# Optimization experiments

Measured on AMD Instinct MI355X. Metric: run time of the kernel, lower is better.

The kernel has to match this reference:

```python
import jax, jax.numpy as jnp
import numpy as np

STRIDE = 4
EPS = 1e-12  # guards sqrt grad at exactly-zero distance (weight[0] is all zeros)


def rbf_conv(x, w, stride=STRIDE):
    # x: (N, 1, H, W); w: (O, kh, kw). Computes per-window cdist to all O
    # prototype filters, then gauss RBF with std = unbiased std of the (N, O)
    # distance matrix at each window position (matches torch.std(dist)).
    O, kh, kw = w.shape
    patches = jax.lax.conv_general_dilated_patches(
        x, (kh, kw), (stride, stride), 'VALID')      # (N, kh*kw, oh, ow)
    p = jnp.transpose(patches, (0, 2, 3, 1))          # (N, oh, ow, P)
    wf = w.reshape(O, -1)                              # (O, P)
    d2 = (jnp.sum(p * p, -1)[..., None] + jnp.sum(wf * wf, -1)
          - 2.0 * jnp.einsum('nhwp,op->nhwo', p, wf))
    dist = jnp.sqrt(jnp.maximum(d2, 0.0) + EPS)       # (N, oh, ow, O)
    std = jnp.std(dist, axis=(0, 3), ddof=1, keepdims=True)  # per window pos
    out = jnp.exp(-0.5 * (dist / std) ** 2)           # gauss RBF
    return jnp.transpose(out, (0, 3, 1, 2))           # (N, O, oh, ow)


def crelu(x, b):
    return x * (x >= b).astype(x.dtype)


def sfm(x, shape, next_kernel, filt, alpha0=0.9):
    # get_RM: (N, C, h_in, w_in) -> (B, h, w, C) regrouping, then alpha-weighted
    # patch pooling over `filt`, emitting (B*h'*w', 1, kh_next, kw_next).
    h, w = shape
    f0, f1 = filt
    C = x.shape[1]
    rm = jnp.transpose(x, (0, 2, 3, 1)).reshape(-1, h, w, C)
    seq = jnp.arange(f0 * f1, dtype=x.dtype)[::-1]       # flipped sequence
    alpha = jnp.tile((alpha0 ** seq).reshape(f0, f1), (h // f0, w // f1))
    out = rm * alpha[None, :, :, None]
    out = out.reshape(-1, h // f0, f0, w // f1, f1, C).mean(axis=(2, 4))
    return out.reshape(-1, 1, *next_kernel)


def channel_forward(xc, w1, w2, w3, w4, cb):
    y = rbf_conv(xc, w1)                       # (B, 100, 6, 6)
    y = crelu(y, cb[0])
    y = sfm(y, (6, 6), (10, 10), (2, 2))       # (B*9, 1, 10, 10)
    y = rbf_conv(y, w2)                        # (B*9, 225, 1, 1)
    y = crelu(y, cb[1])
    y = sfm(y, (3, 3), (15, 15), (1, 3))       # (B*3, 1, 15, 15)
    y = rbf_conv(y, w3)                        # (B*3, 625, 1, 1)
    y = crelu(y, cb[2])
    y = sfm(y, (3, 1), (25, 25), (3, 1))       # (B, 1, 25, 25)
    y = rbf_conv(y, w4)                        # (B, 1225, 1, 1)
    y = crelu(y, cb[3])
    return y


def forward(x, w1, w2, w3, w4, fc_w, fc_b, crelu_bias):
    B = x.shape[0]
    feats = [channel_forward(x[:, c:c + 1], w1[c], w2[c], w3[c], w4[c], crelu_bias)
             for c in range(x.shape[1])]        # fixed loop over 3 color channels
    out = jnp.concatenate(feats, axis=1).reshape(B, -1)  # (B, 3*1225)
    return out @ fc_w.T + fc_b


def setup_inputs() -> dict:
    key = jax.random.key(0)
    ks = jax.random.split(key, 8)

    def kaiming_u(k, shape):
        fan_in = int(np.prod(shape[2:]))        # 1*kh*kw, matches torch
        bound = float(np.sqrt(1.0 / fan_in))    # kaiming_uniform(a=sqrt(5))
        w = jax.random.uniform(k, shape, jnp.float32, -bound, bound)
        return w.at[:, 0].set(0.0)              # torch init zeros filter 0

    B = 4096
    return {
        'x': jax.random.uniform(ks[0], (B, 3, 28, 28), jnp.float32),
        'w1': kaiming_u(ks[1], (3, 100, 5, 5)),
        'w2': kaiming_u(ks[2], (3, 225, 10, 10)),
        'w3': kaiming_u(ks[3], (3, 625, 15, 15)),
        'w4': kaiming_u(ks[4], (3, 1225, 25, 25)),
        'fc_w': jax.random.normal(ks[5], (10, 3 * 1225), jnp.float32) * 0.016,
        'fc_b': jnp.zeros((10,), jnp.float32),
        'crelu_bias': jnp.array([0.4, 0.1, 0.01, 0.01], jnp.float32),
    }


def reference(x, w1, w2, w3, w4, fc_w, fc_b, crelu_bias):
    return forward(x, w1, w2, w3, w4, fc_w, fc_b, crelu_bias)
```

## Files before the change

### kernel.cpp

```cpp
#include <hip/hip_runtime.h>


typedef unsigned short u16;
typedef short bf16x8 __attribute__((ext_vector_type(8)));
typedef float f32x4 __attribute__((ext_vector_type(4)));
typedef unsigned int u32;
typedef u32 u32x4 __attribute__((ext_vector_type(4)));

#define STRIPES 64
#define ACC_L2 0
#define ACC_L3 128
#define ACC_L4 256
#define ACC_TOTAL 384

__device__ __forceinline__ u16 f2bf(float f) {
  unsigned int u = __float_as_uint(f);
  unsigned int r = (u + 0x7fffu + ((u >> 16) & 1u)) >> 16;
  return (u16)r;
}
__device__ __forceinline__ float bf2f(u16 h) {
  return __uint_as_float(((unsigned int)h) << 16);
}
__device__ __forceinline__ u32 cvtpk_bf16(float a, float b) {
  u32 r;
  asm("v_cvt_pk_bf16_f32 %0, %1, %2" : "=v"(r) : "v"(a), "v"(b));
  return r;
}
__device__ __forceinline__ float fexp(float x) { return __expf(x); }
__device__ __forceinline__ float fsqrt(float x) { return __builtin_amdgcn_sqrtf(x); }
__device__ __forceinline__ void gload16(const void* g, const void* l) {
  __builtin_amdgcn_global_load_lds(
      (const __attribute__((address_space(1))) unsigned int*)g,
      (__attribute__((address_space(3))) unsigned int*)l, 16, 0, 0);
}

__global__ void zero_acc_kernel(double* __restrict__ acc, int n) {
  int i = blockIdx.x * blockDim.x + threadIdx.x;
  if (i < n) acc[i] = 0.0;
}

__global__ __launch_bounds__(128) void w_prep(
    const float* __restrict__ W, int O, int K, int Opad, int Kp,
    u16* __restrict__ hi, u16* __restrict__ lo, float* __restrict__ wn)
{
  __shared__ float red[2];
  int o = blockIdx.x, cc = blockIdx.y, t = threadIdx.x;
  const float* src = W + ((size_t)cc * O + o) * K;
  u16* dh = hi + ((size_t)cc * Opad + o) * Kp;
  u16* dl = lo + ((size_t)cc * Opad + o) * Kp;
  float p = 0.f;
  for (int k = t; k < Kp; k += 128) {
    float v = (o < O && k < K) ? src[k] : 0.f;
    u16 h = f2bf(v);
    u16 l = f2bf(v - bf2f(h));
    dh[k] = h; dl[k] = l;
    p = fmaf(v, v, p);
  }
  for (int off = 32; off; off >>= 1) p += __shfl_down(p, off, 64);
  if ((t & 63) == 0) red[t >> 6] = p;
  __syncthreads();
  if (t == 0) wn[(size_t)cc * Opad + o] = red[0] + red[1];
}

__global__ __launch_bounds__(256) void l1_gemm_d2(
    const float* __restrict__ x, int c0,
    const u16* __restrict__ W1h, const u16* __restrict__ W1l,
    const float* __restrict__ w1n, float* __restrict__ dist1, int sD1c,
    float* __restrict__ part, int sPartc, int NBLK)
{
  __shared__ __align__(16) u16 sm[16384];
  __shared__ float img[1568];
  __shared__ float pnsm[512];
  __shared__ float pnloc[128];
  const int t = threadIdx.x;
  const int w = t >> 6, lane = t & 63;
  const int b0 = blockIdx.x * 2;
  const int zi = blockIdx.y, c = c0 + zi;
  const u16* Wh = W1h + (size_t)c * 4096;
  const u16* Wl = W1l + (size_t)c * 4096;
  const float* wn = w1n + (size_t)c * 128;
  dist1 += (size_t)zi * sD1c;
  part  += (size_t)zi * sPartc;

  {
    const int kk = (w & 3) * 8;
#pragma unroll
    for (int u = 0; u < 2; ++u) {
      const size_t gb = (size_t)(u * 64 + lane) * 32 + kk;
      const int ls = ((w & 3) * 128 + u * 64) * 8;
      gload16(Wh + gb, sm + 8192 + ls);
      gload16(Wl + gb, sm + 12288 + ls);
    }
  }
#pragma unroll
  for (int im = 0; im < 2; ++im) {
    if (t < 196)
      ((float4*)(img + im * 784))[t] =
          ((const float4*)(x + ((size_t)(b0 + im) * 3 + c) * 784))[t];
  }
  __syncthreads();
  for (int s = t; s < 512; s += 256) {
    int q = s >> 7, row = s & 127;
    int im = row >> 6, pr = row & 63;
    int pi = pr / 6, pj = pr - pi * 6;
    const float* ib = img + im * 784 + pi * 4 * 28 + pj * 4;
    float v[8]; float pn = 0.f;
#pragma unroll
    for (int e = 0; e < 8; ++e) {
      int k = q * 8 + e;
      float val = 0.f;
      if (pr < 36 && k < 25) { int r = k / 5, ss = k - r * 5; val = ib[r * 28 + ss]; }
      v[e] = val; pn = fmaf(val, val, pn);
    }
    u32x4 hp, lp;
#pragma unroll
    for (int e = 0; e < 4; ++e) {
      u32 h = cvtpk_bf16(v[2 * e], v[2 * e + 1]);
      float l0 = v[2 * e]     - __uint_as_float(h << 16);
      float l1 = v[2 * e + 1] - __uint_as_float(h & 0xffff0000u);
      hp[e] = h;
      lp[e] = cvtpk_bf16(l0, l1);
    }
    *(u32x4*)(sm + (q * 128 + row) * 8) = hp;
    *(u32x4*)(sm + 4096 + (q * 128 + row) * 8) = lp;
    pnsm[s] = pn;
  }
  asm volatile("s_waitcnt vmcnt(0)" ::: "memory");
  __syncthreads();
  if (t < 128) pnloc[t] = pnsm[t] + pnsm[128 + t] + pnsm[256 + t] + pnsm[384 + t];

  const int wr = w >> 1, wc = w & 1;
  const int q4 = lane >> 4, r16 = lane & 15;
  f32x4 accv[4][4];
#pragma unroll
  for (int i = 0; i < 4; ++i)
#pragma unroll
    for (int j = 0; j < 4; ++j) accv[i][j] = (f32x4){0.f, 0.f, 0.f, 0.f};

  bf16x8 Ah[4], Al[4], Bh[4], Bl[4];
#pragma unroll
  for (int i = 0; i < 4; ++i) {
    int ao = (q4 * 128 + wr * 64 + i * 16 + r16) * 8;
    int bo = (q4 * 128 + wc * 64 + i * 16 + r16) * 8;
    Ah[i] = *(const bf16x8*)(sm + ao);
    Al[i] = *(const bf16x8*)(sm + 4096 + ao);
    Bh[i] = *(const bf16x8*)(sm + 8192 + bo);
    Bl[i] = *(const bf16x8*)(sm + 12288 + bo);
  }
#pragma unroll
  for (int j = 0; j < 4; ++j) {
#pragma unroll
    for (int i = 0; i < 4; ++i)
      accv[i][j] = __builtin_amdgcn_mfma_f32_16x16x32_bf16(Ah[i], Bh[j], accv[i][j], 0, 0, 0);
#pragma unroll
    for (int i = 0; i < 4; ++i)
      accv[i][j] = __builtin_amdgcn_mfma_f32_16x16x32_bf16(Al[i], Bh[j], accv[i][j], 0, 0, 0);
#pragma unroll
    for (int i = 0; i < 4; ++i)
      accv[i][j] = __builtin_amdgcn_mfma_f32_16x16x32_bf16(Ah[i], Bl[j], accv[i][j], 0, 0, 0);
  }
  __syncthreads();

  float* smf = (float*)sm;
  int colv[4]; float wnv[4];
#pragma unroll
  for (int j = 0; j < 4; ++j) {
    colv[j] = wc * 64 + j * 16 + r16;
    wnv[j] = (colv[j] < 100) ? wn[colv[j]] : 0.f;
  }
#pragma unroll
  for (int i = 0; i < 4; ++i) {
#pragma unroll
    for (int r = 0; r < 4; ++r) {
      int pos = i * 16 + q4 * 4 + r;
      if (pos < 36) {
        float pn = pnloc[wr * 64 + pos];
        float* drow = dist1 + ((size_t)(b0 + wr) * 36 + pos) * 100;
        float sl = 0.f, ql = 0.f;
#pragma unroll
        for (int j = 0; j < 4; ++j) {
          if (colv[j] < 100) {
            float d2 = pn + wnv[j] - 2.f * accv[i][j][r];
            float d2c = fmaxf(d2, 0.f) + 1e-12f;
            drow[colv[j]] = d2c;
            sl += fsqrt(d2c); ql += d2c;
          }
        }
        smf[pos * 66 + w * 16 + r16] = sl;
        smf[(36 + pos) * 66 + w * 16 + r16] = ql;
      }
    }
  }
  __syncthreads();
  if (t < 72) {
    const float* row = smf + (size_t)t * 66;
    float v0 = 0.f;
#pragma unroll
    for (int k = 0; k < 64; ++k) v0 += row[k];
    part[(size_t)t * NBLK + blockIdx.x] = v0;
  }
}

__global__ __launch_bounds__(256) void l1_part_fin(
    const float* __restrict__ part, int sPartc, float* __restrict__ inv36, int sInvc,
    double n, int NBLK)
{
  __shared__ double sh[8];
  int pos = blockIdx.x, zi = blockIdx.y, t = threadIdx.x;
  part += (size_t)zi * sPartc; inv36 += (size_t)zi * sInvc;
  double s = 0.0, q = 0.0;
  for (int b = t; b < NBLK; b += 256) {
    s += part[(size_t)pos * NBLK + b];
    q += part[(size_t)(36 + pos) * NBLK + b];
  }
  for (int off = 32; off; off >>= 1) {
    s += __shfl_down(s, off, 64);
    q += __shfl_down(q, off, 64);
  }
  if ((t & 63) == 0) { sh[(t >> 6) * 2] = s; sh[(t >> 6) * 2 + 1] = q; }
  __syncthreads();
  if (t == 0) {
    s = sh[0] + sh[2] + sh[4] + sh[6];
    q = sh[1] + sh[3] + sh[5] + sh[7];
    double var = (q - s * s / n) / (n - 1.0);
    inv36[pos] = var > 0.0 ? (float)(0.5 / var) : __builtin_inff();
  }
}

__global__ __launch_bounds__(128) void l1_sfm_lite(
    const float* __restrict__ d1, int sD1c,
    const float* __restrict__ inv36, int sInvc, const float* __restrict__ cb,
    u16* __restrict__ Xhi, u16* __restrict__ Xlo, float* __restrict__ xn,
    int sXc, int sxnc)
{
  __shared__ float inv_s[36];
  __shared__ float xnsm[9][2];
  int b = blockIdx.x, zi = blockIdx.y, t = threadIdx.x;
  d1 += (size_t)zi * sD1c; inv36 += (size_t)zi * sInvc;
  Xhi += (size_t)zi * sXc; Xlo += (size_t)zi * sXc; xn += (size_t)zi * sxnc;
  if (t < 36) inv_s[t] = inv36[t];
  __syncthreads();
  const float* db = d1 + (size_t)b * 3600;
  float bias = cb[0];
  int wv = t >> 6;
#pragma unroll
  for (int IJ = 0; IJ < 9; ++IJ) {
    const int I = IJ / 3, J = IJ - I * 3;
    const int p00 = 12 * I + 2 * J;
    float v = 0.f;
    if (t < 100) {
      float e00 = fexp(-db[p00 * 100 + t] * inv_s[p00]);
      float e01 = fexp(-db[(p00 + 1) * 100 + t] * inv_s[p00 + 1]);
      float e10 = fexp(-db[(p00 + 6) * 100 + t] * inv_s[p00 + 6]);
      float e11 = fexp(-db[(p00 + 7) * 100 + t] * inv_s[p00 + 7]);
      e00 = (e00 >= bias) ? e00 : 0.f;
      e01 = (e01 >= bias) ? e01 : 0.f;
      e10 = (e10 >= bias) ? e10 : 0.f;
      e11 = (e11 >= bias) ? e11 : 0.f;
      v = 0.25f * (fmaf(0.729f, e00, 0.81f * e01) + fmaf(0.9f, e10, e11));
    }
    size_t xrow = (size_t)b * 9 + IJ;
    u16 h = f2bf(v);
    u16 l = f2bf(v - bf2f(h));
    Xhi[xrow * 128 + t] = h;
    Xlo[xrow * 128 + t] = l;
    float p = v * v;
    for (int off = 32; off; off >>= 1) p += __shfl_down(p, off, 64);
    if ((t & 63) == 0) xnsm[IJ][wv] = p;
  }
  __syncthreads();
  if (t < 9) xn[(size_t)b * 9 + t] = xnsm[t][0] + xnsm[t][1];
}

__global__ __launch_bounds__(512, 2) void gemm_dist_pipe(
    const u16* __restrict__ Xhi, const u16* __restrict__ Xlo,
    const u16* __restrict__ Whi, const u16* __restrict__ Wlo,
    const float* __restrict__ xn, const float* __restrict__ wn,
    float* __restrict__ dist, int O, int Kp,
    double* __restrict__ acc, int accbase, int c0,
    int sXc, int sWc, int sxnc, int swnc, int sdistc)
{
  __shared__ __align__(16) u16 sm[65536];
  int zi = blockIdx.z, c = c0 + zi;
  Xhi += (size_t)zi * sXc; Xlo += (size_t)zi * sXc;
  Whi += (size_t)c * sWc;  Wlo += (size_t)c * sWc;
  xn += (size_t)zi * sxnc; wn += (size_t)c * swnc;
  dist += (size_t)zi * sdistc;
  acc += (size_t)c * ACC_TOTAL;

  const int t = threadIdx.x;
  const int w = t >> 6, lane = t & 63;
  const int wr = w >> 1, wc = w & 1;
  const int sq = w & 3, half = w >> 2;
  const int m0 = blockIdx.x * 256, o0 = blockIdx.y * 256;
  const int q4 = lane >> 4, r16 = lane & 15;
  const int nsteps = Kp / 32;

  f32x4 accv[4][8];
#pragma unroll
  for (int i = 0; i < 4; ++i)
#pragma unroll
    for (int j = 0; j < 8; ++j) accv[i][j] = (f32x4){0.f, 0.f, 0.f, 0.f};

  auto stageA = [&](int buf, int ks) {
    const int kk = ks * 32 + sq * 8;
    u16* base = sm + buf * 32768;
#pragma unroll
    for (int u = 0; u < 2; ++u) {
      const int row = half * 128 + u * 64 + lane;
      const size_t ga = (size_t)(m0 + row) * Kp + kk;
      const int ls = (sq * 256 + half * 128 + u * 64) * 8;
      gload16(Xhi + ga, base + ls);
      gload16(Xlo + ga, base + 8192 + ls);
    }
  };
  auto stageB = [&](int buf, int ks) {
    const int kk = ks * 32 + sq * 8;
    u16* base = sm + buf * 32768;
#pragma unroll
    for (int u = 0; u < 2; ++u) {
      const int row = half * 128 + u * 64 + lane;
      const size_t gb = (size_t)(o0 + row) * Kp + kk;
      const int ls = (sq * 256 + half * 128 + u * 64) * 8;
      gload16(Whi + gb, base + 16384 + ls);
      gload16(Wlo + gb, base + 24576 + ls);
    }
  };

  stageA(0, 0);
  stageB(0, 0);
  for (int ks = 0; ks < nsteps; ++ks) {
    const u16* base = sm + (ks & 1) * 32768;
    asm volatile("s_waitcnt vmcnt(2)\n\ts_barrier" ::: "memory");
    if (ks + 1 < nsteps) stageA((ks + 1) & 1, ks + 1);

    bf16x8 Ah[4], Al[4];
#pragma unroll
    for (int i = 0; i < 4; ++i) {
      int ao = (q4 * 256 + wr * 64 + i * 16 + r16) * 8;
      Ah[i] = *(const bf16x8*)(base + ao);
      Al[i] = *(const bf16x8*)(base + 8192 + ao);
    }
    __builtin_amdgcn_s_setprio(1);
#pragma unroll
    for (int j = 0; j < 4; ++j) {
      int bo = (q4 * 256 + wc * 128 + j * 16 + r16) * 8;
      bf16x8 Bh = *(const bf16x8*)(base + 16384 + bo);
      bf16x8 Bl = *(const bf16x8*)(base + 24576 + bo);
#pragma unroll
      for (int i = 0; i < 4; ++i)
        accv[i][j] = __builtin_amdgcn_mfma_f32_16x16x32_bf16(Ah[i], Bh, accv[i][j], 0, 0, 0);
#pragma unroll
      for (int i = 0; i < 4; ++i)
        accv[i][j] = __builtin_amdgcn_mfma_f32_16x16x32_bf16(Al[i], Bh, accv[i][j], 0, 0, 0);
#pragma unroll
      for (int i = 0; i < 4; ++i)
        accv[i][j] = __builtin_amdgcn_mfma_f32_16x16x32_bf16(Ah[i], Bl, accv[i][j], 0, 0, 0);
    }
    __builtin_amdgcn_s_setprio(0);

    if (ks + 1 < nsteps) {
      asm volatile("s_waitcnt vmcnt(4)\n\ts_barrier" ::: "memory");
      stageB((ks + 1) & 1, ks + 1);
    } else {
      asm volatile("s_waitcnt vmcnt(0)\n\ts_barrier" ::: "memory");
    }
    __builtin_amdgcn_s_setprio(1);
#pragma unroll
    for (int j = 4; j < 8; ++j) {
      int bo = (q4 * 256 + wc * 128 + j * 16 + r16) * 8;
      bf16x8 Bh = *(const bf16x8*)(base + 16384 + bo);
      bf16x8 Bl = *(const bf16x8*)(base + 24576 + bo);
#pragma unroll
      for (int i = 0; i < 4; ++i)
        accv[i][j] = __builtin_amdgcn_mfma_f32_16x16x32_bf16(Ah[i], Bh, accv[i][j], 0, 0, 0);
#pragma unroll
      for (int i = 0; i < 4; ++i)
        accv[i][j] = __builtin_amdgcn_mfma_f32_16x16x32_bf16(Al[i], Bh, accv[i][j], 0, 0, 0);
#pragma unroll
      for (int i = 0; i < 4; ++i)
        accv[i][j] = __builtin_amdgcn_mfma_f32_16x16x32_bf16(Ah[i], Bl, accv[i][j], 0, 0, 0);
    }
    __builtin_amdgcn_s_setprio(0);
  }

  double s = 0.0, qd = 0.0;
#pragma unroll
  for (int i = 0; i < 4; ++i) {
    const int mb = m0 + wr * 64 + i * 16 + q4 * 4;
    float xnv[4];
#pragma unroll
    for (int r = 0; r < 4; ++r) xnv[r] = xn[mb + r];
    float sf = 0.f, qf = 0.f;
#pragma unroll
    for (int j = 0; j < 8; ++j) {
      const int o = o0 + wc * 128 + j * 16 + r16;
      if (o < O) {
        const float wnv = wn[o];
#pragma unroll
        for (int r = 0; r < 4; ++r) {
          float d2 = xnv[r] + wnv - 2.f * accv[i][j][r];
          float d2c = fmaxf(d2, 0.f) + 1e-12f;
          dist[(size_t)(mb + r) * O + o] = d2c;
          sf += fsqrt(d2c); qf += d2c;
        }
      }
    }
    s += sf; qd += qf;
  }
  for (int off = 32; off; off >>= 1) {
    s += __shfl_down(s, off, 64);
    qd += __shfl_down(qd, off, 64);
  }
  double* redsm = (double*)(sm + (nsteps & 1) * 32768);
  if (lane == 0) { redsm[w * 2] = s; redsm[w * 2 + 1] = qd; }
  __syncthreads();
  if (t == 0) {
    s = 0.0; qd = 0.0;
#pragma unroll
    for (int ww = 0; ww < 8; ++ww) { s += redsm[ww * 2]; qd += redsm[ww * 2 + 1]; }
    int stripe = (blockIdx.x + blockIdx.y * gridDim.x) & (STRIPES - 1);
    atomicAdd(&acc[accbase + stripe * 2], s);
    atomicAdd(&acc[accbase + stripe * 2 + 1], qd);
  }
}

__device__ __forceinline__ float block_inv_from_acc(
    const double* __restrict__ acc, int base, double n, float* sh)
{
  __syncthreads();
  int t = threadIdx.x;
  if (t < 64) {
    double s = acc[base + 2 * t], q = acc[base + 2 * t + 1];
    for (int off = 32; off; off >>= 1) {
      s += __shfl_down(s, off, 64);
      q += __shfl_down(q, off, 64);
    }
    if (t == 0) {
      double var = (q - s * s / n) / (n - 1.0);
      *sh = var > 0.0 ? (float)(0.5 / var) : __builtin_inff();
    }
  }
  __syncthreads();
  return *sh;
}

__global__ __launch_bounds__(256) void l2_sfm(
    const float* __restrict__ dist2, const double* __restrict__ acc, double n,
    const float* __restrict__ cb, u16* __restrict__ Xhi, u16* __restrict__ Xlo,
    float* __restrict__ xn, int c0, int sdistc, int sXc, int sxnc)
{
  __shared__ float shinv;
  __shared__ float red[4];
  int zi = blockIdx.z, c = c0 + zi;
  dist2 += (size_t)zi * sdistc;
  Xhi += (size_t)zi * sXc; Xlo += (size_t)zi * sXc; xn += (size_t)zi * sxnc;
  float inv = block_inv_from_acc(acc + (size_t)c * ACC_TOTAL, ACC_L2, n, &shinv);
  int b = blockIdx.x, u = blockIdx.y, ch = threadIdx.x;
  float bias = cb[1];
  float v = 0.f;
  if (ch < 225) {
    const float av[3] = {0.81f, 0.9f, 1.0f};
    float a = 0.f;
#pragma unroll
    for (int vv = 0; vv < 3; ++vv) {
      float d2 = dist2[((size_t)b * 9 + u * 3 + vv) * 225 + ch];
      float e = fexp(-d2 * inv);
      e = (e >= bias) ? e : 0.f;
      a = fmaf(e, av[vv], a);
    }
    v = a * (1.f / 3.f);
  }
  size_t row = (size_t)b * 3 + u;
  u16 h = f2bf(v);
  u16 l = f2bf(v - bf2f(h));
  Xhi[row * 256 + ch] = h;
  Xlo[row * 256 + ch] = l;
  float p = v * v;
  for (int off = 32; off; off >>= 1) p += __shfl_down(p, off, 64);
  if ((ch & 63) == 0) red[ch >> 6] = p;
  __syncthreads();
  if (ch == 0) xn[row] = red[0] + red[1] + red[2] + red[3];
}

__global__ __launch_bounds__(256) void l3_sfm(
    const float* __restrict__ dist3, const double* __restrict__ acc, double n,
    const float* __restrict__ cb, u16* __restrict__ Xhi, u16* __restrict__ Xlo,
    float* __restrict__ xn, int c0, int sdistc, int sXc, int sxnc)
{
  __shared__ float shinv;
  __shared__ float red[4];
  int zi = blockIdx.y, c = c0 + zi;
  dist3 += (size_t)zi * sdistc;
  Xhi += (size_t)zi * sXc; Xlo += (size_t)zi * sXc; xn += (size_t)zi * sxnc;
  float inv = block_inv_from_acc(acc + (size_t)c * ACC_TOTAL, ACC_L3, n, &shinv);
  int b = blockIdx.x, t = threadIdx.x;
  float bias = cb[2];
  const float au[3] = {0.81f, 0.9f, 1.0f};
  float p = 0.f;
  for (int ch = t; ch < 640; ch += 256) {
    float v = 0.f;
    if (ch < 625) {
      float a = 0.f;
#pragma unroll
      for (int u = 0; u < 3; ++u) {
        float d2 = dist3[((size_t)b * 3 + u) * 625 + ch];
        float e = fexp(-d2 * inv);
        e = (e >= bias) ? e : 0.f;
        a = fmaf(e, au[u], a);
      }
      v = a * (1.f / 3.f);
    }
    u16 h = f2bf(v);
    u16 l = f2bf(v - bf2f(h));
    Xhi[(size_t)b * 640 + ch] = h;
    Xlo[(size_t)b * 640 + ch] = l;
    p = fmaf(v, v, p);
  }
  for (int off = 32; off; off >>= 1) p += __shfl_down(p, off, 64);
  if ((t & 63) == 0) red[t >> 6] = p;
  __syncthreads();
  if (t == 0) xn[b] = red[0] + red[1] + red[2] + red[3];
}

__global__ __launch_bounds__(128) void fc_acc(
    const float* __restrict__ dist4, const double* __restrict__ acc, double n,
    const float* __restrict__ cb, const float* __restrict__ fcw,
    const float* __restrict__ fcb, float* __restrict__ out,
    int c0, int nc, int sdistc)
{
  __shared__ float shinv;
  int b = blockIdx.x, t = threadIdx.x;
  float bias = cb[3];
  float p[10];
#pragma unroll
  for (int k = 0; k < 10; ++k) p[k] = 0.f;
  for (int zi = 0; zi < nc; ++zi) {
    int c = c0 + zi;
    float inv = block_inv_from_acc(acc + (size_t)c * ACC_TOTAL, ACC_L4, n, &shinv);
    const float* d4 = dist4 + (size_t)zi * sdistc;
    for (int j = t; j < 1225; j += 128) {
      float d2 = d4[(size_t)b * 1225 + j];
      float v = fexp(-d2 * inv);
      v = (v >= bias) ? v : 0.f;
#pragma unroll
      for (int k = 0; k < 10; ++k) p[k] = fmaf(v, fcw[k * 3675 + c * 1225 + j], p[k]);
    }
  }
#pragma unroll
  for (int k = 0; k < 10; ++k)
    for (int off = 32; off; off >>= 1) p[k] += __shfl_down(p[k], off, 64);
  __shared__ float red[2][10];
  int wave = t >> 6;
  if ((t & 63) == 0) {
#pragma unroll
    for (int k = 0; k < 10; ++k) red[wave][k] = p[k];
  }
  __syncthreads();
  if (t < 10) {
    float v = red[0][t] + red[1][t];
    if (c0 == 0) out[(size_t)b * 10 + t] = fcb[t] + v;
    else         out[(size_t)b * 10 + t] += v;
  }
}

extern "C" void kernel_launch(void* const* d_in, const int* in_sizes, int n_in,
                              void* d_out, int out_size, void* d_ws, size_t ws_size,
                              hipStream_t stream) {
  const float* x   = (const float*)d_in[0];
  const float* w1  = (const float*)d_in[1];
  const float* w2  = (const float*)d_in[2];
  const float* w3  = (const float*)d_in[3];
  const float* w4  = (const float*)d_in[4];
  const float* fcw = (const float*)d_in[5];
  const float* fcb = (const float*)d_in[6];
  const float* cb  = (const float*)d_in[7];
  float* out = (float*)d_out;
  const int B = in_sizes[0] / (3 * 28 * 28);
  const int M2 = B * 9, M3 = B * 3;
  const int NB = B / 2;

  const size_t W2SZ = 256 * 128, W3SZ = 768 * 256, W4SZ = (size_t)1280 * 640;
  const size_t WTOT = 3 * (W2SZ + W3SZ + W4SZ);

  int tier;
  u16 *Xbase, *Whi, *Wlo, *W1h, *W1l;
  float *wn, *w1n, *xn, *inv36, *part;
  double* accd;
  float* Sf;
  for (tier = 0; tier < 3; ++tier) {
    size_t cur = 0;
    char* basep = (char*)d_ws;
    auto take = [&](size_t bytes) {
      void* r = basep + cur;
      cur = (cur + bytes + 255) & ~(size_t)255;
      return r;
    };
    int nc = (tier <= 1) ? 3 : 1;
    int ncL1 = (tier == 0) ? 3 : 1;
    size_t Ssz = (size_t)M2 * 225 * 4 * nc;
    size_t d1sz = (size_t)B * 3600 * 4 * ncL1;
    if (d1sz > Ssz) Ssz = d1sz;
    Sf = (float*)take(Ssz);
    Xbase = (u16*)take((size_t)M2 * 128 * 2 * 2 * nc);
    Whi = (u16*)take(WTOT * 2); Wlo = (u16*)take(WTOT * 2);
    W1h = (u16*)take(12288 * 2); W1l = (u16*)take(12288 * 2);
    wn  = (float*)take(3 * (256 + 768 + 1280) * 4);
    w1n = (float*)take(384 * 4);
    xn    = (float*)take((size_t)M2 * 4 * nc);
    inv36 = (float*)take(40 * 4 * ncL1);
    part  = (float*)take((size_t)72 * NB * 4 * ncL1);
    accd  = (double*)take(3 * ACC_TOTAL * 8);
    if (cur <= ws_size || tier == 2) break;
  }
  const int nc = (tier <= 1) ? 3 : 1;
  const bool batL1 = (tier == 0);

  const int sX2c   = (nc == 3) ? M2 * 128 * 2 : 0;
  const int sX3c   = (nc == 3) ? M3 * 256 * 2 : 0;
  const int sX4c   = (nc == 3) ? B * 640 * 2 : 0;
  const int sD2c   = (nc == 3) ? M2 * 225 : 0;
  const int sD3c   = (nc == 3) ? M3 * 625 : 0;
  const int sD4c   = (nc == 3) ? B * 1225 : 0;
  const int sXn2c  = (nc == 3) ? M2 : 0;
  const int sXn3c  = (nc == 3) ? M3 : 0;
  const int sXn4c  = (nc == 3) ? B : 0;
  const int sD1c   = batL1 ? B * 3600 : 0;
  const int sPartc = batL1 ? 72 * NB : 0;
  const int sInvL1 = batL1 ? 40 : 0;

  u16* x2hi = Xbase;   u16* x2lo = Xbase + (size_t)M2 * 128;
  u16* x3hi = Xbase;   u16* x3lo = Xbase + (size_t)M3 * 256;
  u16* x4hi = Xbase;   u16* x4lo = Xbase + (size_t)B * 640;
  u16* Whi2 = Whi;                 u16* Wlo2 = Wlo;                 float* wn2 = wn;
  u16* Whi3 = Whi + 3 * W2SZ;      u16* Wlo3 = Wlo + 3 * W2SZ;      float* wn3 = wn + 3 * 256;
  u16* Whi4 = Whi + 3 * (W2SZ + W3SZ); u16* Wlo4 = Wlo + 3 * (W2SZ + W3SZ);
  float* wn4 = wn + 3 * (256 + 768);

  zero_acc_kernel<<<(3 * ACC_TOTAL + 255) / 256, 256, 0, stream>>>(accd, 3 * ACC_TOTAL);
  w_prep<<<dim3(128, 3),  128, 0, stream>>>(w1, 100, 25,  128, 32,  W1h,  W1l,  w1n);
  w_prep<<<dim3(256, 3),  128, 0, stream>>>(w2, 225, 100, 256, 128, Whi2, Wlo2, wn2);
  w_prep<<<dim3(768, 3),  128, 0, stream>>>(w3, 625, 225, 768, 256, Whi3, Wlo3, wn3);
  w_prep<<<dim3(1280, 3), 128, 0, stream>>>(w4, 1225, 625, 1280, 640, Whi4, Wlo4, wn4);

  for (int c0 = 0; c0 < 3; c0 += nc) {
    if (batL1) {
      l1_gemm_d2<<<dim3(NB, 3), 256, 0, stream>>>(x, 0, W1h, W1l, w1n, Sf, sD1c,
                                                  part, sPartc, NB);
      l1_part_fin<<<dim3(36, 3), 256, 0, stream>>>(part, sPartc, inv36, sInvL1,
                                                   (double)B * 100.0, NB);
      l1_sfm_lite<<<dim3(B, 3), 128, 0, stream>>>(
          Sf, sD1c, inv36, sInvL1, cb, x2hi, x2lo, xn, sX2c, sXn2c);
    } else {
      for (int ci = 0; ci < nc; ++ci) {
        int c = c0 + ci;
        l1_gemm_d2<<<dim3(NB, 1), 256, 0, stream>>>(x, c, W1h, W1l, w1n, Sf, 0,
                                                    part, 0, NB);
        l1_part_fin<<<dim3(36, 1), 256, 0, stream>>>(part, 0, inv36, 0,
                                                     (double)B * 100.0, NB);
        l1_sfm_lite<<<dim3(B, 1), 128, 0, stream>>>(
            Sf, 0, inv36, 0, cb, x2hi + (size_t)ci * sX2c, x2lo + (size_t)ci * sX2c,
            xn + (size_t)ci * sXn2c, 0, 0);
      }
    }

    gemm_dist_pipe<<<dim3(M2 / 256, 1, nc), 512, 0, stream>>>(
        x2hi, x2lo, Whi2, Wlo2, xn, wn2, Sf, 225, 128, accd, ACC_L2, c0,
        sX2c, (int)W2SZ, sXn2c, 256, sD2c);
    l2_sfm<<<dim3(B, 3, nc), 256, 0, stream>>>(
        Sf, accd, (double)M2 * 225.0, cb, x3hi, x3lo, xn, c0, sD2c, sX3c, sXn3c);

    gemm_dist_pipe<<<dim3(M3 / 256, 3, nc), 512, 0, stream>>>(
        x3hi, x3lo, Whi3, Wlo3, xn, wn3, Sf, 625, 256, accd, ACC_L3, c0,
        sX3c, (int)W3SZ, sXn3c, 768, sD3c);
    l3_sfm<<<dim3(B, nc), 256, 0, stream>>>(
        Sf, accd, (double)M3 * 625.0, cb, x4hi, x4lo, xn, c0, sD3c, sX4c, sXn4c);

    gemm_dist_pipe<<<dim3(B / 256, 5, nc), 512, 0, stream>>>(
        x4hi, x4lo, Whi4, Wlo4, xn, wn4, Sf, 1225, 640, accd, ACC_L4, c0,
        sX4c, (int)W4SZ, sXn4c, 1280, sD4c);
    fc_acc<<<B, 128, 0, stream>>>(
        Sf, accd, (double)B * 1225.0, cb, fcw, fcb, out, c0, nc, sD4c);
  }
}
```

Measured before the change: 482.4 us.

## Split GEMM k-step into four barrier-synced phases interleaving loads and MFMAs

Restructures the main k-loop of the split-bf16 GEMM into four phases. Each phase loads two B fragments from LDS, issues one quarter of the next step's global-to-LDS staging, and runs 24 MFMAs, with explicit lgkmcnt waits and sched_barriers between. The aim is to spread global loads and LDS reads evenly across the MFMA work, a ping-pong style schedule. In exchange it adds extra s_barriers per k-step, and forcing lgkmcnt(0) before the MFMAs may stall on LDS reads.

```diff
diff --git a/kernel.cpp b/kernel.cpp
--- a/kernel.cpp
+++ b/kernel.cpp
@@ -302,86 +302,88 @@
 #pragma unroll
     for (int j = 0; j < 8; ++j) accv[i][j] = (f32x4){0.f, 0.f, 0.f, 0.f};
 
-  auto stageA = [&](int buf, int ks) {
+  auto stageA_u = [&](int buf, int ks, int u) {
     const int kk = ks * 32 + sq * 8;
     u16* base = sm + buf * 32768;
-#pragma unroll
-    for (int u = 0; u < 2; ++u) {
-      const int row = half * 128 + u * 64 + lane;
-      const size_t ga = (size_t)(m0 + row) * Kp + kk;
-      const int ls = (sq * 256 + half * 128 + u * 64) * 8;
-      gload16(Xhi + ga, base + ls);
-      gload16(Xlo + ga, base + 8192 + ls);
-    }
+    const int row = half * 128 + u * 64 + lane;
+    const size_t ga = (size_t)(m0 + row) * Kp + kk;
+    const int ls = (sq * 256 + half * 128 + u * 64) * 8;
+    gload16(Xhi + ga, base + ls);
+    gload16(Xlo + ga, base + 8192 + ls);
   };
-  auto stageB = [&](int buf, int ks) {
+  auto stageB_u = [&](int buf, int ks, int u) {
     const int kk = ks * 32 + sq * 8;
     u16* base = sm + buf * 32768;
-#pragma unroll
-    for (int u = 0; u < 2; ++u) {
-      const int row = half * 128 + u * 64 + lane;
-      const size_t gb = (size_t)(o0 + row) * Kp + kk;
-      const int ls = (sq * 256 + half * 128 + u * 64) * 8;
-      gload16(Whi + gb, base + 16384 + ls);
-      gload16(Wlo + gb, base + 24576 + ls);
-    }
+    const int row = half * 128 + u * 64 + lane;
+    const size_t gb = (size_t)(o0 + row) * Kp + kk;
+    const int ls = (sq * 256 + half * 128 + u * 64) * 8;
+    gload16(Whi + gb, base + 16384 + ls);
+    gload16(Wlo + gb, base + 24576 + ls);
   };
 
-  stageA(0, 0);
-  stageB(0, 0);
+  stageA_u(0, 0, 0); stageA_u(0, 0, 1);
+  stageB_u(0, 0, 0); stageB_u(0, 0, 1);
+
   for (int ks = 0; ks < nsteps; ++ks) {
     const u16* base = sm + (ks & 1) * 32768;
-    asm volatile("s_waitcnt vmcnt(2)\n\ts_barrier" ::: "memory");
-    if (ks + 1 < nsteps) stageA((ks + 1) & 1, ks + 1);
-
+    const int nb = (ks + 1) & 1;
+    const bool more = (ks + 1 < nsteps);
     bf16x8 Ah[4], Al[4];
-#pragma unroll
-    for (int i = 0; i < 4; ++i) {
-      int ao = (q4 * 256 + wr * 64 + i * 16 + r16) * 8;
-      Ah[i] = *(const bf16x8*)(base + ao);
-      Al[i] = *(const bf16x8*)(base + 8192 + ao);
-    }
-    __builtin_amdgcn_s_setprio(1);
-#pragma unroll
-    for (int j = 0; j < 4; ++j) {
-      int bo = (q4 * 256 + wc * 128 + j * 16 + r16) * 8;
-      bf16x8 Bh = *(const bf16x8*)(base + 16384 + bo);
-      bf16x8 Bl = *(const bf16x8*)(base + 24576 + bo);
+
+#pragma unroll
+    for (int ph = 0; ph < 4; ++ph) {
+      if (ph == 0) {
+        asm volatile("s_waitcnt vmcnt(2)\n\ts_barrier" ::: "memory");
+      } else if (ph == 2) {
+        if (more) asm volatile("s_waitcnt vmcnt(4)\n\ts_barrier" ::: "memory");
+        else      asm volatile("s_waitcnt vmcnt(0)\n\ts_barrier" ::: "memory");
+      } else {
+        __builtin_amdgcn_s_barrier();
+      }
+      if (ph == 0) {
+#pragma unroll
+        for (int i = 0; i < 4; ++i) {
+          int ao = (q4 * 256 + wr * 64 + i * 16 + r16) * 8;
+          Ah[i] = *(const bf16x8*)(base + ao);
+          Al[i] = *(const bf16x8*)(base + 8192 + ao);
+        }
+      }
+      const int j0 = ph * 2;
+      int bo0 = (q4 * 256 + wc * 128 + j0 * 16 + r16) * 8;
+      int bo1 = (q4 * 256 + wc * 128 + (j0 + 1) * 16 + r16) * 8;
+      bf16x8 Bh0 = *(const bf16x8*)(base + 16384 + bo0);
+      bf16x8 Bl0 = *(const bf16x8*)(base + 24576 + bo0);
+      bf16x8 Bh1 = *(const bf16x8*)(base + 16384 + bo1);
+      bf16x8 Bl1 = *(const bf16x8*)(base + 24576 + bo1);
+      if (more) {
+        if (ph == 0)      stageA_u(nb, ks + 1, 0);
+        else if (ph == 1) stageA_u(nb, ks + 1, 1);
+        else if (ph == 2) stageB_u(nb, ks + 1, 0);
+        else              stageB_u(nb, ks + 1, 1);
+      }
+      asm volatile("s_waitcnt lgkmcnt(0)" ::: "memory");
+      __builtin_amdgcn_sched_barrier(0);
+      __builtin_amdgcn_s_setprio(1);
 #pragma unroll
       for (int i = 0; i < 4; ++i)
-        accv[i][j] = __builtin_amdgcn_mfma_f32_16x16x32_bf16(Ah[i], Bh, accv[i][j], 0, 0, 0);
+        accv[i][j0] = __builtin_amdgcn_mfma_f32_16x16x32_bf16(Ah[i], Bh0, accv[i][j0], 0, 0, 0);
 #pragma unroll
       for (int i = 0; i < 4; ++i)
-        accv[i][j] = __builtin_amdgcn_mfma_f32_16x16x32_bf16(Al[i], Bh, accv[i][j], 0, 0, 0);
+        accv[i][j0] = __builtin_amdgcn_mfma_f32_16x16x32_bf16(Al[i], Bh0, accv[i][j0], 0, 0, 0);
 #pragma unroll
       for (int i = 0; i < 4; ++i)
-        accv[i][j] = __builtin_amdgcn_mfma_f32_16x16x32_bf16(Ah[i], Bl, accv[i][j], 0, 0, 0);
-    }
-    __builtin_amdgcn_s_setprio(0);
-
-    if (ks + 1 < nsteps) {
-      asm volatile("s_waitcnt vmcnt(4)\n\ts_barrier" ::: "memory");
-      stageB((ks + 1) & 1, ks + 1);
-    } else {
-      asm volatile("s_waitcnt vmcnt(0)\n\ts_barrier" ::: "memory");
-    }
-    __builtin_amdgcn_s_setprio(1);
-#pragma unroll
-    for (int j = 4; j < 8; ++j) {
-      int bo = (q4 * 256 + wc * 128 + j * 16 + r16) * 8;
-      bf16x8 Bh = *(const bf16x8*)(base + 16384 + bo);
-      bf16x8 Bl = *(const bf16x8*)(base + 24576 + bo);
+        accv[i][j0] = __builtin_amdgcn_mfma_f32_16x16x32_bf16(Ah[i], Bl0, accv[i][j0], 0, 0, 0);
 #pragma unroll
       for (int i = 0; i < 4; ++i)
-        accv[i][j] = __builtin_amdgcn_mfma_f32_16x16x32_bf16(Ah[i], Bh, accv[i][j], 0, 0, 0);
+        accv[i][j0 + 1] = __builtin_amdgcn_mfma_f32_16x16x32_bf16(Ah[i], Bh1, accv[i][j0 + 1], 0, 0, 0);
 #pragma unroll
       for (int i = 0; i < 4; ++i)
-        accv[i][j] = __builtin_amdgcn_mfma_f32_16x16x32_bf16(Al[i], Bh, accv[i][j], 0, 0, 0);
+        accv[i][j0 + 1] = __builtin_amdgcn_mfma_f32_16x16x32_bf16(Al[i], Bh1, accv[i][j0 + 1], 0, 0, 0);
 #pragma unroll
       for (int i = 0; i < 4; ++i)
-        accv[i][j] = __builtin_amdgcn_mfma_f32_16x16x32_bf16(Ah[i], Bl, accv[i][j], 0, 0, 0);
-    }
-    __builtin_amdgcn_s_setprio(0);
+        accv[i][j0 + 1] = __builtin_amdgcn_mfma_f32_16x16x32_bf16(Ah[i], Bl1, accv[i][j0 + 1], 0, 0, 0);
+      __builtin_amdgcn_s_setprio(0);
+    }
   }
 
   double s = 0.0, qd = 0.0;
```

After: 479.7 us. Within noise of the previous version (-0.5%).

## Halve GEMM tile to 128x128 and merge weight-prep launches into one kernel

Applied to the files above, without the earlier changes.

The distance GEMM moves from 256x256 tiles to 128x128 tiles with half the LDS and a single combined A/B staging step per k-iteration. Launch bounds go from 2 to 4 blocks per CU, and grids are enlarged to match. The aim is more blocks in flight and better load balance across CUs, at the cost of less data reuse per tile, more global/L2 traffic, and a simpler overlap between loads and MFMA. Separately, zeroing the accumulators and the four weight-prep launches are merged into one kernel to cut launch overhead.

```diff
diff --git a/kernel.cpp b/kernel.cpp
--- a/kernel.cpp
+++ b/kernel.cpp
@@ -34,17 +34,31 @@
       (__attribute__((address_space(3))) unsigned int*)l, 16, 0, 0);
 }
 
-__global__ void zero_acc_kernel(double* __restrict__ acc, int n) {
-  int i = blockIdx.x * blockDim.x + threadIdx.x;
-  if (i < n) acc[i] = 0.0;
-}
-
-__global__ __launch_bounds__(128) void w_prep(
-    const float* __restrict__ W, int O, int K, int Opad, int Kp,
-    u16* __restrict__ hi, u16* __restrict__ lo, float* __restrict__ wn)
+__global__ __launch_bounds__(128) void prep_all(
+    const float* __restrict__ w1, const float* __restrict__ w2,
+    const float* __restrict__ w3, const float* __restrict__ w4,
+    u16* __restrict__ W1h, u16* __restrict__ W1l,
+    u16* __restrict__ Whi2, u16* __restrict__ Wlo2,
+    u16* __restrict__ Whi3, u16* __restrict__ Wlo3,
+    u16* __restrict__ Whi4, u16* __restrict__ Wlo4,
+    float* __restrict__ w1n, float* __restrict__ wn2,
+    float* __restrict__ wn3, float* __restrict__ wn4,
+    double* __restrict__ accd, int naccd)
 {
   __shared__ float red[2];
-  int o = blockIdx.x, cc = blockIdx.y, t = threadIdx.x;
+  int bid = blockIdx.x, t = threadIdx.x;
+  if (bid < 9) {
+    int i = bid * 128 + t;
+    if (i < naccd) accd[i] = 0.0;
+    return;
+  }
+  bid -= 9;
+  const float* W; u16 *hi, *lo; float* wn; int O, K, Opad, Kp;
+  if (bid < 384)        { W = w1; hi = W1h;  lo = W1l;  wn = w1n; O = 100;  K = 25;  Opad = 128;  Kp = 32;  }
+  else if (bid < 1152)  { bid -= 384;  W = w2; hi = Whi2; lo = Wlo2; wn = wn2; O = 225;  K = 100; Opad = 256;  Kp = 128; }
+  else if (bid < 3456)  { bid -= 1152; W = w3; hi = Whi3; lo = Wlo3; wn = wn3; O = 625;  K = 225; Opad = 768;  Kp = 256; }
+  else                  { bid -= 3456; W = w4; hi = Whi4; lo = Wlo4; wn = wn4; O = 1225; K = 625; Opad = 1280; Kp = 640; }
+  int o = bid % Opad, cc = bid / Opad;
   const float* src = W + ((size_t)cc * O + o) * K;
   u16* dh = hi + ((size_t)cc * Opad + o) * Kp;
   u16* dl = lo + ((size_t)cc * Opad + o) * Kp;
@@ -272,7 +286,7 @@
   if (t < 9) xn[(size_t)b * 9 + t] = xnsm[t][0] + xnsm[t][1];
 }
 
-__global__ __launch_bounds__(512, 2) void gemm_dist_pipe(
+__global__ __launch_bounds__(512, 4) void gemm_dist_pipe(
     const u16* __restrict__ Xhi, const u16* __restrict__ Xlo,
     const u16* __restrict__ Whi, const u16* __restrict__ Wlo,
     const float* __restrict__ xn, const float* __restrict__ wn,
@@ -280,7 +294,7 @@
     double* __restrict__ acc, int accbase, int c0,
     int sXc, int sWc, int sxnc, int swnc, int sdistc)
 {
-  __shared__ __align__(16) u16 sm[65536];
+  __shared__ __align__(16) u16 sm[32768];
   int zi = blockIdx.z, c = c0 + zi;
   Xhi += (size_t)zi * sXc; Xlo += (size_t)zi * sXc;
   Whi += (size_t)c * sWc;  Wlo += (size_t)c * sWc;
@@ -292,109 +306,75 @@
   const int w = t >> 6, lane = t & 63;
   const int wr = w >> 1, wc = w & 1;
   const int sq = w & 3, half = w >> 2;
-  const int m0 = blockIdx.x * 256, o0 = blockIdx.y * 256;
+  const int m0 = blockIdx.x * 128, o0 = blockIdx.y * 128;
   const int q4 = lane >> 4, r16 = lane & 15;
   const int nsteps = Kp / 32;
 
-  f32x4 accv[4][8];
-#pragma unroll
-  for (int i = 0; i < 4; ++i)
-#pragma unroll
-    for (int j = 0; j < 8; ++j) accv[i][j] = (f32x4){0.f, 0.f, 0.f, 0.f};
-
-  auto stageA = [&](int buf, int ks) {
+  f32x4 accv[2][4];
+#pragma unroll
+  for (int i = 0; i < 2; ++i)
+#pragma unroll
+    for (int j = 0; j < 4; ++j) accv[i][j] = (f32x4){0.f, 0.f, 0.f, 0.f};
+
+  auto stage = [&](int buf, int ks) {
     const int kk = ks * 32 + sq * 8;
-    u16* base = sm + buf * 32768;
-#pragma unroll
-    for (int u = 0; u < 2; ++u) {
-      const int row = half * 128 + u * 64 + lane;
-      const size_t ga = (size_t)(m0 + row) * Kp + kk;
-      const int ls = (sq * 256 + half * 128 + u * 64) * 8;
-      gload16(Xhi + ga, base + ls);
-      gload16(Xlo + ga, base + 8192 + ls);
-    }
+    u16* base = sm + buf * 16384;
+    const int row = half * 64 + lane;
+    const size_t ga = (size_t)(m0 + row) * Kp + kk;
+    const size_t gb = (size_t)(o0 + row) * Kp + kk;
+    const int ls = (sq * 128 + row) * 8;
+    gload16(Xhi + ga, base + ls);
+    gload16(Xlo + ga, base + 4096 + ls);
+    gload16(Whi + gb, base + 8192 + ls);
+    gload16(Wlo + gb, base + 12288 + ls);
   };
-  auto stageB = [&](int buf, int ks) {
-    const int kk = ks * 32 + sq * 8;
-    u16* base = sm + buf * 32768;
-#pragma unroll
-    for (int u = 0; u < 2; ++u) {
-      const int row = half * 128 + u * 64 + lane;
-      const size_t gb = (size_t)(o0 + row) * Kp + kk;
-      const int ls = (sq * 256 + half * 128 + u * 64) * 8;
-      gload16(Whi + gb, base + 16384 + ls);
-      gload16(Wlo + gb, base + 24576 + ls);
-    }
-  };
-
-  stageA(0, 0);
-  stageB(0, 0);
+
+  stage(0, 0);
   for (int ks = 0; ks < nsteps; ++ks) {
-    const u16* base = sm + (ks & 1) * 32768;
-    asm volatile("s_waitcnt vmcnt(2)\n\ts_barrier" ::: "memory");
-    if (ks + 1 < nsteps) stageA((ks + 1) & 1, ks + 1);
-
-    bf16x8 Ah[4], Al[4];
-#pragma unroll
-    for (int i = 0; i < 4; ++i) {
-      int ao = (q4 * 256 + wr * 64 + i * 16 + r16) * 8;
+    const u16* base = sm + (ks & 1) * 16384;
+    const bool more = (ks + 1 < nsteps);
+    if (more) stage((ks + 1) & 1, ks + 1);
+    if (more) asm volatile("s_waitcnt vmcnt(4)\n\ts_barrier" ::: "memory");
+    else      asm volatile("s_waitcnt vmcnt(0)\n\ts_barrier" ::: "memory");
+
+    bf16x8 Ah[2], Al[2];
+#pragma unroll
+    for (int i = 0; i < 2; ++i) {
+      int ao = (q4 * 128 + wr * 32 + i * 16 + r16) * 8;
       Ah[i] = *(const bf16x8*)(base + ao);
-      Al[i] = *(const bf16x8*)(base + 8192 + ao);
+      Al[i] = *(const bf16x8*)(base + 4096 + ao);
     }
     __builtin_amdgcn_s_setprio(1);
 #pragma unroll
     for (int j = 0; j < 4; ++j) {
-      int bo = (q4 * 256 + wc * 128 + j * 16 + r16) * 8;
-      bf16x8 Bh = *(const bf16x8*)(base + 16384 + bo);
-      bf16x8 Bl = *(const bf16x8*)(base + 24576 + bo);
-#pragma unroll
-      for (int i = 0; i < 4; ++i)
+      int bo = (q4 * 128 + wc * 64 + j * 16 + r16) * 8;
+      bf16x8 Bh = *(const bf16x8*)(base + 8192 + bo);
+      bf16x8 Bl = *(const bf16x8*)(base + 12288 + bo);
+#pragma unroll
+      for (int i = 0; i < 2; ++i)
         accv[i][j] = __builtin_amdgcn_mfma_f32_16x16x32_bf16(Ah[i], Bh, accv[i][j], 0, 0, 0);
 #pragma unroll
-      for (int i = 0; i < 4; ++i)
+      for (int i = 0; i < 2; ++i)
         accv[i][j] = __builtin_amdgcn_mfma_f32_16x16x32_bf16(Al[i], Bh, accv[i][j], 0, 0, 0);
 #pragma unroll
-      for (int i = 0; i < 4; ++i)
+      for (int i = 0; i < 2; ++i)
         accv[i][j] = __builtin_amdgcn_mfma_f32_16x16x32_bf16(Ah[i], Bl, accv[i][j], 0, 0, 0);
     }
     __builtin_amdgcn_s_setprio(0);
-
-    if (ks + 1 < nsteps) {
-      asm volatile("s_waitcnt vmcnt(4)\n\ts_barrier" ::: "memory");
-      stageB((ks + 1) & 1, ks + 1);
-    } else {
-      asm volatile("s_waitcnt vmcnt(0)\n\ts_barrier" ::: "memory");
-    }
-    __builtin_amdgcn_s_setprio(1);
-#pragma unroll
-    for (int j = 4; j < 8; ++j) {
-      int bo = (q4 * 256 + wc * 128 + j * 16 + r16) * 8;
-      bf16x8 Bh = *(const bf16x8*)(base + 16384 + bo);
-      bf16x8 Bl = *(const bf16x8*)(base + 24576 + bo);
-#pragma unroll
-      for (int i = 0; i < 4; ++i)
-        accv[i][j] = __builtin_amdgcn_mfma_f32_16x16x32_bf16(Ah[i], Bh, accv[i][j], 0, 0, 0);
-#pragma unroll
-      for (int i = 0; i < 4; ++i)
-        accv[i][j] = __builtin_amdgcn_mfma_f32_16x16x32_bf16(Al[i], Bh, accv[i][j], 0, 0, 0);
-#pragma unroll
-      for (int i = 0; i < 4; ++i)
-        accv[i][j] = __builtin_amdgcn_mfma_f32_16x16x32_bf16(Ah[i], Bl, accv[i][j], 0, 0, 0);
-    }
-    __builtin_amdgcn_s_setprio(0);
+    asm volatile("s_barrier" ::: "memory");
   }
 
   double s = 0.0, qd = 0.0;
 #pragma unroll
-  for (int i = 0; i < 4; ++i) {
-    const int mb = m0 + wr * 64 + i * 16 + q4 * 4;
+  for (int i = 0; i < 2; ++i) {
+    const int mb = m0 + wr * 32 + i * 16 + q4 * 4;
     float xnv[4];
 #pragma unroll
     for (int r = 0; r < 4; ++r) xnv[r] = xn[mb + r];
     float sf = 0.f, qf = 0.f;
 #pragma unroll
-    for (int j = 0; j < 8; ++j) {
-      const int o = o0 + wc * 128 + j * 16 + r16;
+    for (int j = 0; j < 4; ++j) {
+      const int o = o0 + wc * 64 + j * 16 + r16;
       if (o < O) {
         const float wnv = wn[o];
 #pragma unroll
@@ -412,7 +392,7 @@
     s += __shfl_down(s, off, 64);
     qd += __shfl_down(qd, off, 64);
   }
-  double* redsm = (double*)(sm + (nsteps & 1) * 32768);
+  double* redsm = (double*)(sm + (nsteps & 1) * 16384);
   if (lane == 0) { redsm[w * 2] = s; redsm[w * 2 + 1] = qd; }
   __syncthreads();
   if (t == 0) {
@@ -637,11 +617,9 @@
   u16* Whi4 = Whi + 3 * (W2SZ + W3SZ); u16* Wlo4 = Wlo + 3 * (W2SZ + W3SZ);
   float* wn4 = wn + 3 * (256 + 768);
 
-  zero_acc_kernel<<<(3 * ACC_TOTAL + 255) / 256, 256, 0, stream>>>(accd, 3 * ACC_TOTAL);
-  w_prep<<<dim3(128, 3),  128, 0, stream>>>(w1, 100, 25,  128, 32,  W1h,  W1l,  w1n);
-  w_prep<<<dim3(256, 3),  128, 0, stream>>>(w2, 225, 100, 256, 128, Whi2, Wlo2, wn2);
-  w_prep<<<dim3(768, 3),  128, 0, stream>>>(w3, 625, 225, 768, 256, Whi3, Wlo3, wn3);
-  w_prep<<<dim3(1280, 3), 128, 0, stream>>>(w4, 1225, 625, 1280, 640, Whi4, Wlo4, wn4);
+  prep_all<<<9 + 384 + 768 + 2304 + 3840, 128, 0, stream>>>(
+      w1, w2, w3, w4, W1h, W1l, Whi2, Wlo2, Whi3, Wlo3, Whi4, Wlo4,
+      w1n, wn2, wn3, wn4, accd, 3 * ACC_TOTAL);
 
   for (int c0 = 0; c0 < 3; c0 += nc) {
     if (batL1) {
@@ -664,19 +642,19 @@
       }
     }
 
-    gemm_dist_pipe<<<dim3(M2 / 256, 1, nc), 512, 0, stream>>>(
+    gemm_dist_pipe<<<dim3(M2 / 128, 2, nc), 512, 0, stream>>>(
         x2hi, x2lo, Whi2, Wlo2, xn, wn2, Sf, 225, 128, accd, ACC_L2, c0,
         sX2c, (int)W2SZ, sXn2c, 256, sD2c);
     l2_sfm<<<dim3(B, 3, nc), 256, 0, stream>>>(
         Sf, accd, (double)M2 * 225.0, cb, x3hi, x3lo, xn, c0, sD2c, sX3c, sXn3c);
 
-    gemm_dist_pipe<<<dim3(M3 / 256, 3, nc), 512, 0, stream>>>(
+    gemm_dist_pipe<<<dim3(M3 / 128, 6, nc), 512, 0, stream>>>(
         x3hi, x3lo, Whi3, Wlo3, xn, wn3, Sf, 625, 256, accd, ACC_L3, c0,
         sX3c, (int)W3SZ, sXn3c, 768, sD3c);
     l3_sfm<<<dim3(B, nc), 256, 0, stream>>>(
         Sf, accd, (double)M3 * 625.0, cb, x4hi, x4lo, xn, c0, sD3c, sX4c, sXn4c);
 
-    gemm_dist_pipe<<<dim3(B / 256, 5, nc), 512, 0, stream>>>(
+    gemm_dist_pipe<<<dim3(B / 128, 10, nc), 512, 0, stream>>>(
         x4hi, x4lo, Whi4, Wlo4, xn, wn4, Sf, 1225, 640, accd, ACC_L4, c0,
         sX4c, (int)W4SZ, sXn4c, 1280, sD4c);
     fc_acc<<<B, 128, 0, stream>>>(
```

New measurement: 529.9 us. +9.9%, slower.
